# Performance work log

Measured on AMD Instinct MI355X. Metric: run time of the kernel, lower is better.

## Reference

```python
import jax, jax.numpy as jnp
import numpy as np

PH = PW = 5  # roi_size
EPS = 1e-5


def _conv1x1(x, w, b):
    # x: (B,Cin,H,W), w: (Cout,Cin)
    return jnp.einsum('bchw,oc->bohw', x, w) + b[None, :, None, None]


def _resize_ac(x, oh, ow):
    # F.interpolate bilinear, align_corners=True. x: (B,C,H,W)
    B, C, H, W = x.shape
    ys = jnp.linspace(0.0, H - 1.0, oh)
    xs = jnp.linspace(0.0, W - 1.0, ow)
    y0 = jnp.floor(ys).astype(jnp.int32); y1 = jnp.minimum(y0 + 1, H - 1)
    x0 = jnp.floor(xs).astype(jnp.int32); x1 = jnp.minimum(x0 + 1, W - 1)
    ly = (ys - y0)[:, None]; lx = (xs - x0)[None, :]
    v00 = x[:, :, y0[:, None], x0[None, :]]
    v01 = x[:, :, y0[:, None], x1[None, :]]
    v10 = x[:, :, y1[:, None], x0[None, :]]
    v11 = x[:, :, y1[:, None], x1[None, :]]
    return v00 * (1 - ly) * (1 - lx) + v01 * (1 - ly) * lx + v10 * ly * (1 - lx) + v11 * ly * lx


def _roi_align_one(feat, box):
    # torchvision RoIAlign, spatial_scale=1, sampling_ratio=1, aligned=False
    # feat: (C,H,W), box: (x1,y1,x2,y2)
    C, H, W = feat.shape
    bx1, by1, bx2, by2 = box[0], box[1], box[2], box[3]
    rw = jnp.maximum(bx2 - bx1, 1.0)
    rh = jnp.maximum(by2 - by1, 1.0)
    xs = bx1 + (jnp.arange(PW, dtype=feat.dtype) + 0.5) * (rw / PW)
    ys = by1 + (jnp.arange(PH, dtype=feat.dtype) + 0.5) * (rh / PH)
    yg = jnp.broadcast_to(ys[:, None], (PH, PW))
    xg = jnp.broadcast_to(xs[None, :], (PH, PW))
    valid = (yg >= -1.0) & (yg <= H) & (xg >= -1.0) & (xg <= W)
    y = jnp.clip(yg, 0.0, H - 1.0); x = jnp.clip(xg, 0.0, W - 1.0)
    y0 = jnp.floor(y).astype(jnp.int32); x0 = jnp.floor(x).astype(jnp.int32)
    y1i = jnp.minimum(y0 + 1, H - 1); x1i = jnp.minimum(x0 + 1, W - 1)
    ly = y - y0; lx = x - x0
    v = (feat[:, y0, x0] * (1 - ly) * (1 - lx) + feat[:, y0, x1i] * (1 - ly) * lx
         + feat[:, y1i, x0] * ly * (1 - lx) + feat[:, y1i, x1i] * ly * lx)
    return v * valid  # (C,PH,PW)


def _layernorm(x, w, b):
    mu = jnp.mean(x, -1, keepdims=True)
    var = jnp.var(x, -1, keepdims=True)
    return (x - mu) * jax.lax.rsqrt(var + EPS) * w + b


def setup_inputs() -> dict:
    key = jax.random.key(0)
    ks = jax.random.split(key, 16)
    B, G, NB, HF = 8, 8, 16, 28
    x4 = jax.random.normal(ks[0], (B, 1024, 14, 14), jnp.float32)
    x5 = jax.random.normal(ks[1], (B, 2048, 7, 7), jnp.float32)
    bx = jax.random.uniform(ks[2], (B, NB), minval=0.0, maxval=18.0)
    by = jax.random.uniform(ks[3], (B, NB), minval=0.0, maxval=18.0)
    bw = jax.random.uniform(ks[4], (B, NB), minval=3.0, maxval=10.0)
    bh = jax.random.uniform(ks[5], (B, NB), minval=3.0, maxval=10.0)
    boxes = jnp.stack([bx, by, jnp.minimum(bx + bw, 28.0), jnp.minimum(by + bh, 28.0)], -1)
    group = jax.random.randint(ks[6], (B, G, 2), 0, NB, jnp.int32)
    real_in_num = jnp.full((B,), G, jnp.int32)
    label_s = jax.random.randint(ks[7], (B, G), 0, 6, jnp.int64)
    label_s = jnp.where(jnp.arange(G)[None, :] % 3 == 0, -1, label_s)  # exercise both branches
    skeleton = jax.random.normal(ks[8], (B, G, HF, HF), jnp.float32)
    D = 1536 * PH * PW  # 38400
    return {
        'x4': x4, 'x5': x5, 'boxes': boxes, 'skeleton': skeleton,
        'group': group, 'real_in_num': real_in_num, 'label_s': label_s,
        'conv1_w': jax.random.normal(ks[9], (), jnp.float32) * 0.5,
        'conv1_b': jax.random.normal(ks[10], (), jnp.float32) * 0.1,
        'conv2_w': jax.random.normal(ks[11], (512, 1024), jnp.float32) * 0.03,
        'conv2_b': jnp.zeros((512,), jnp.float32),
        'conv3_w': jax.random.normal(ks[12], (1024, 2048), jnp.float32) * 0.02,
        'conv3_b': jnp.zeros((1024,), jnp.float32),
        'norm1_w': jnp.ones((D,), jnp.float32), 'norm1_b': jnp.zeros((D,), jnp.float32),
        'norm2_w': jnp.ones((512,), jnp.float32), 'norm2_b': jnp.zeros((512,), jnp.float32),
        'fc1_w': jax.random.normal(ks[13], (512, D), jnp.float32) * float(np.sqrt(2.0 / D)),
        'fc1_b': jnp.zeros((512,), jnp.float32),
        'fc2_w': jax.random.normal(ks[14], (6, 512), jnp.float32) * float(np.sqrt(2.0 / 512)),
        'fc2_b': jnp.zeros((6,), jnp.float32),
    }


def reference(x4, x5, boxes, skeleton, group, real_in_num, label_s,
              conv1_w, conv1_b, conv2_w, conv2_b, conv3_w, conv3_b,
              norm1_w, norm1_b, norm2_w, norm2_b, fc1_w, fc1_b, fc2_w, fc2_b):
    B, G = skeleton.shape[0], skeleton.shape[1]
    HF, WF = skeleton.shape[2], skeleton.shape[3]
    # backbone heads: 1x1 conv + bilinear upsample (align_corners=True), concat
    f4 = _resize_ac(_conv1x1(x4, conv2_w, conv2_b), HF, WF)   # (B,512,28,28)
    f5 = _resize_ac(_conv1x1(x5, conv3_w, conv3_b), HF, WF)   # (B,1024,28,28)
    app = jnp.concatenate([f4, f5], axis=1)                   # (B,1536,28,28)
    C = app.shape[1]
    # per-person pose gate: 1x1 conv (scalar on single channel) + sigmoid
    gate = jax.nn.sigmoid(skeleton * conv1_w + conv1_b)       # (B,G,28,28)
    gated = gate[:, :, None] * app[:, None]                   # (B,G,C,28,28)
    use_gate = (label_s != -1)[:, :, None, None, None]
    pose_feature = jnp.where(use_gate, gated, app[:, None])   # (B,G,C,28,28)
    # union box of the two interacting people (get_box_tensor)
    bidx = jnp.arange(B)[:, None]
    b1 = boxes[bidx, group[..., 0]]                           # (B,G,4)
    b2 = boxes[bidx, group[..., 1]]
    ub = jnp.stack([jnp.minimum(b1[..., 0], b2[..., 0]), jnp.minimum(b1[..., 1], b2[..., 1]),
                    jnp.maximum(b1[..., 2], b2[..., 2]), jnp.maximum(b1[..., 3], b2[..., 3])], -1)
    # batched RoIAlign over all N = B*G boxes
    feats = pose_feature.reshape(B * G, C, HF, WF)
    rois = jax.vmap(_roi_align_one)(feats, ub.reshape(B * G, 4))  # (N,C,5,5)
    sk = rois.reshape(B * G, -1)                              # (N,38400)
    sk = jax.nn.relu(_layernorm(sk, norm1_w, norm1_b))
    # dropout(p=0.9) is identity in eval mode
    sk = sk @ fc1_w.T + fc1_b
    sk = _layernorm(sk, norm2_w, norm2_b)
    score = sk @ fc2_w.T + fc2_b                              # (N,6)
    return score
```

## Files before the change

### kernel.cpp

```cpp
#include <hip/hip_runtime.h>
#include <math.h>

#define B8   8
#define HW4  196
#define HW5  49
#define HFW  28
#define NPIX 784
#define CAPP 1536
#define D1   38400
#define NR   64

typedef short short8 __attribute__((ext_vector_type(8)));
typedef short short4v __attribute__((ext_vector_type(4)));
typedef float floatx16 __attribute__((ext_vector_type(16)));

__device__ __forceinline__ unsigned short f2bf(float f) {
  unsigned u = __float_as_uint(f);
  u += 0x7FFF + ((u >> 16) & 1);
  return (unsigned short)(u >> 16);
}

struct Params {
  const float *x4, *x5, *boxes, *skel;
  const int *group, *label;
  const float *c1w, *c1b, *w2c, *b2c, *w3c, *b3c;
  const float *n1w, *n1b, *n2w, *n2b, *fw1, *fb1, *fw2, *fb2;
  float* out;
  unsigned short *x4T, *x5T, *sknT;
  float *f4T, *f5T, *tap4w, *tap5w, *descw, *roisP, *stats, *out1;
  int *tap4o, *tap5o, *desco;
};

struct Sh0 { float tile[6432]; };
struct GemmSh {
  unsigned short As[4096];
  unsigned short Bs[4096];
};
struct Sh2 {
  float cw4[16], cw5[16], wgs;
  int co4[16], co5[16];
  float red[8];
};
struct Sh3 { float tile[6424]; };
struct Sh5 { float red[8]; float red2[24]; };

__device__ __forceinline__ void gemm_unit(
    GemmSh& sh, const unsigned short* __restrict__ A, const float* __restrict__ Bw,
    float* __restrict__ C, int mt, int nt, int k0, int kchunk,
    int K, int N, int Mvalid, bool accum) {
  int t = threadIdx.x;
  int wave = t >> 6, lane = t & 63;
  int wm = wave & 1, wn = wave >> 1;
  const unsigned short* Aptr = A + (size_t)(mt * 64) * K + k0;
  const float* Bptr = Bw + (size_t)(nt * 64) * K + k0;

  int m0 = t >> 3, ka = (t & 7) * 8, koa = t & 7;
  int n0 = t >> 4, kbo = (t & 15) * 4, kob = (t & 15) >> 1, half = t & 1;

  short8 areg[2];
  float4 breg[4];
  floatx16 acc;
#pragma unroll
  for (int i = 0; i < 16; i++) acc[i] = 0.f;
  int nkb = kchunk >> 6;

  auto LOAD = [&](int j) {
    int kof = j * 64;
    areg[0] = *(const short8*)(Aptr + (size_t)m0 * K + kof + ka);
    areg[1] = *(const short8*)(Aptr + (size_t)(m0 + 32) * K + kof + ka);
#pragma unroll
    for (int i = 0; i < 4; i++)
      breg[i] = *(const float4*)(Bptr + (size_t)(n0 + 16 * i) * K + kof + kbo);
  };
  auto STORE = [&]() {
    *(short8*)&sh.As[koa * 512 + ((m0 ^ koa)) * 8] = areg[0];
    *(short8*)&sh.As[koa * 512 + (((m0 + 32) ^ koa)) * 8] = areg[1];
#pragma unroll
    for (int i = 0; i < 4; i++) {
      short4v v;
      v[0] = (short)f2bf(breg[i].x); v[1] = (short)f2bf(breg[i].y);
      v[2] = (short)f2bf(breg[i].z); v[3] = (short)f2bf(breg[i].w);
      int n = n0 + 16 * i;
      *(short4v*)&sh.Bs[kob * 512 + ((n ^ kob)) * 8 + half * 4] = v;
    }
  };

  LOAD(0);
  STORE();
  __syncthreads();

  for (int kb = 0; kb < nkb; kb++) {
    bool more = (kb + 1) < nkb;
    if (more) LOAD(kb + 1);
#pragma unroll
    for (int s = 0; s < 4; s++) {
      int ko = 2 * s + (lane >> 5);
      int am = wm * 32 + (lane & 31);
      int bn = wn * 32 + (lane & 31);
      short8 af = *(const short8*)&sh.As[ko * 512 + ((am ^ ko)) * 8];
      short8 bf = *(const short8*)&sh.Bs[ko * 512 + ((bn ^ ko)) * 8];
      acc = __builtin_amdgcn_mfma_f32_32x32x16_bf16(af, bf, acc, 0, 0, 0);
    }
    __syncthreads();
    if (more) {
      STORE();
      __syncthreads();
    }
  }

  int col = nt * 64 + wn * 32 + (lane & 31);
  int rbase = mt * 64 + wm * 32 + 4 * (lane >> 5);
  if (accum) {
#pragma unroll
    for (int reg = 0; reg < 16; reg++) {
      int row = rbase + (reg & 3) + 8 * (reg >> 2);
      if (row < Mvalid) atomicAdd(&C[(size_t)row * N + col], acc[reg]);
    }
  } else {
#pragma unroll
    for (int reg = 0; reg < 16; reg++) {
      int row = rbase + (reg & 3) + 8 * (reg >> 2);
      if (row < Mvalid) C[(size_t)row * N + col] = acc[reg];
    }
  }
}

__device__ __forceinline__ float gate_val(const float* sk, int yy, int xx,
                                          float c1w, float c1b, bool use) {
  if (!use) return 1.f;
  float z = sk[yy * HFW + xx] * c1w + c1b;
  return 1.f / (1.f + expf(-z));
}

__global__ __launch_bounds__(256, 4) void k_phase0(Params p) {
  __shared__ Sh0 sh;
  int bid = blockIdx.x, t = threadIdx.x, gb = gridDim.x;
  int gtid = bid * 256 + t;
  int nth = gb * 256;
  float4 z4 = make_float4(0.f, 0.f, 0.f, 0.f);
  for (int i = gtid; i < 319488; i += nth) ((float4*)p.f4T)[i] = z4;
  for (int i = gtid; i < 8192; i += nth) ((float4*)p.out1)[i] = z4;
  if (gtid < 128) p.stats[gtid] = 0.f;

  for (int u = bid; u < 836; u += gb) {
    __syncthreads();
    if (u < 256) {
      int b = u >> 5, cc = u & 31;
      for (int i = t; i < 32 * HW4; i += 256) {
        int c = i / HW4, hw = i - c * HW4;
        sh.tile[c * 201 + hw] = p.x4[((size_t)(b * 1024 + cc * 32 + c)) * HW4 + hw];
      }
      __syncthreads();
      for (int i = t; i < HW4 * 32; i += 256) {
        int hw = i >> 5, c = i & 31;
        p.x4T[((size_t)(b * HW4 + hw)) * 1024 + cc * 32 + c] = f2bf(sh.tile[c * 201 + hw]);
      }
    } else if (u < 768) {
      int u2 = u - 256;
      int b = u2 >> 6, cc = u2 & 63;
      for (int i = t; i < 32 * HW5; i += 256) {
        int c = i / HW5, hw = i - c * HW5;
        sh.tile[c * 51 + hw] = p.x5[((size_t)(b * 2048 + cc * 32 + c)) * HW5 + hw];
      }
      __syncthreads();
      for (int i = t; i < HW5 * 32; i += 256) {
        int hw = i >> 5, c = i & 31;
        p.x5T[((size_t)(b * HW5 + hw)) * 2048 + cc * 32 + c] = f2bf(sh.tile[c * 51 + hw]);
      }
    } else if (u < 832) {
      int bg = u - 768;
      if (t < 25) {
        int b = bg >> 3;
        int i1 = p.group[bg * 2 + 0], i2 = p.group[bg * 2 + 1];
        const float* bb1 = p.boxes + (size_t)(b * 16 + i1) * 4;
        const float* bb2 = p.boxes + (size_t)(b * 16 + i2) * 4;
        float ux1 = fminf(bb1[0], bb2[0]);
        float uy1 = fminf(bb1[1], bb2[1]);
        float ux2 = fmaxf(bb1[2], bb2[2]);
        float uy2 = fmaxf(bb1[3], bb2[3]);
        float rw = fmaxf(ux2 - ux1, 1.0f), rh = fmaxf(uy2 - uy1, 1.0f);
        int iy = t / 5, ix = t % 5;
        float sy = uy1 + (iy + 0.5f) * (rh * 0.2f);
        float sx = ux1 + (ix + 0.5f) * (rw * 0.2f);
        float valid = (sy >= -1.0f && sy <= 28.0f && sx >= -1.0f && sx <= 28.0f) ? 1.f : 0.f;
        float y = fminf(fmaxf(sy, 0.f), 27.f);
        float x = fminf(fmaxf(sx, 0.f), 27.f);
        int y0 = (int)floorf(y), x0 = (int)floorf(x);
        int y1 = min(y0 + 1, 27), x1 = min(x0 + 1, 27);
        float ly = y - (float)y0, lx = x - (float)x0;
        bool use = (p.label[bg] != -1);
        float c1w = p.c1w[0], c1b = p.c1b[0];
        const float* sk = p.skel + (size_t)bg * NPIX;
        int idx = (bg * 25 + t) * 4;
        p.descw[idx + 0] = (1.f - ly) * (1.f - lx) * valid * gate_val(sk, y0, x0, c1w, c1b, use);
        p.descw[idx + 1] = (1.f - ly) * lx * valid * gate_val(sk, y0, x1, c1w, c1b, use);
        p.descw[idx + 2] = ly * (1.f - lx) * valid * gate_val(sk, y1, x0, c1w, c1b, use);
        p.descw[idx + 3] = ly * lx * valid * gate_val(sk, y1, x1, c1w, c1b, use);
        p.desco[idx + 0] = y0 * HFW + x0;
        p.desco[idx + 1] = y0 * HFW + x1;
        p.desco[idx + 2] = y1 * HFW + x0;
        p.desco[idx + 3] = y1 * HFW + x1;
      }
    } else {
      int pix = (u - 832) * 196 + t;
      if (t < 196) {
        int y = pix / HFW, x = pix % HFW;
        {
          float sy = y * (13.0f / 27.0f), sx = x * (13.0f / 27.0f);
          int y0 = (int)sy, x0 = (int)sx;
          int y1 = min(y0 + 1, 13), x1 = min(x0 + 1, 13);
          float ly = sy - y0, lx = sx - x0;
          p.tap4o[pix * 4 + 0] = y0 * 14 + x0; p.tap4w[pix * 4 + 0] = (1.f - ly) * (1.f - lx);
          p.tap4o[pix * 4 + 1] = y0 * 14 + x1; p.tap4w[pix * 4 + 1] = (1.f - ly) * lx;
          p.tap4o[pix * 4 + 2] = y1 * 14 + x0; p.tap4w[pix * 4 + 2] = ly * (1.f - lx);
          p.tap4o[pix * 4 + 3] = y1 * 14 + x1; p.tap4w[pix * 4 + 3] = ly * lx;
        }
        {
          float sy = y * (6.0f / 27.0f), sx = x * (6.0f / 27.0f);
          int y0 = (int)sy, x0 = (int)sx;
          int y1 = min(y0 + 1, 6), x1 = min(x0 + 1, 6);
          float ly = sy - y0, lx = sx - x0;
          p.tap5o[pix * 4 + 0] = y0 * 7 + x0; p.tap5w[pix * 4 + 0] = (1.f - ly) * (1.f - lx);
          p.tap5o[pix * 4 + 1] = y0 * 7 + x1; p.tap5w[pix * 4 + 1] = (1.f - ly) * lx;
          p.tap5o[pix * 4 + 2] = y1 * 7 + x0; p.tap5w[pix * 4 + 2] = ly * (1.f - lx);
          p.tap5o[pix * 4 + 3] = y1 * 7 + x1; p.tap5w[pix * 4 + 3] = ly * lx;
        }
      }
    }
  }
}

__global__ __launch_bounds__(256, 4) void k_phase1(Params p) {
  __shared__ GemmSh sh;
  int bid = blockIdx.x, gb = gridDim.x;
  for (int u = bid; u < 1696; u += gb) {
    __syncthreads();
    if (u < 800) {
      int mt = u % 25, r = u / 25;
      int nt = r & 7, sp = r >> 3;
      gemm_unit(sh, p.x4T, p.w2c, p.f4T, mt, nt, sp * 256, 256, 1024, 512, 1568, true);
    } else {
      int u2 = u - 800;
      int mt = u2 % 7, r = u2 / 7;
      int nt = r & 15, sp = r >> 4;
      gemm_unit(sh, p.x5T, p.w3c, p.f5T, mt, nt, sp * 256, 256, 2048, 1024, 392, true);
    }
  }
}

__global__ __launch_bounds__(256, 4) void k_phase2(Params p) {
  __shared__ Sh2 sh;
  int bid = blockIdx.x, t = threadIdx.x, gb = gridDim.x;
  for (int u = bid; u < 1600; u += gb) {
    __syncthreads();
    int pp = u % 25, bg = u / 25, b = bg >> 3;
    int di = (bg * 25 + pp) * 4;
    if (t < 16) {
      int i = t >> 2, j = t & 3;
      float wg = p.descw[di + i];
      int pix = p.desco[di + i];
      sh.cw4[t] = wg * p.tap4w[pix * 4 + j];
      sh.co4[t] = (b * HW4 + p.tap4o[pix * 4 + j]) * 512;
      sh.cw5[t] = wg * p.tap5w[pix * 4 + j];
      sh.co5[t] = (b * HW5 + p.tap5o[pix * 4 + j]) * 1024;
    }
    if (t == 16) sh.wgs = p.descw[di] + p.descw[di + 1] + p.descw[di + 2] + p.descw[di + 3];
    __syncthreads();
    float w4r[16], w5r[16];
    int o4r[16], o5r[16];
    float wg = sh.wgs;
#pragma unroll
    for (int i = 0; i < 16; i++) {
      w4r[i] = sh.cw4[i]; o4r[i] = sh.co4[i];
      w5r[i] = sh.cw5[i]; o5r[i] = sh.co5[i];
    }
    float ls = 0.f, ls2 = 0.f;
    float* outp = p.roisP + (size_t)(bg * 25 + pp) * CAPP;
    for (int c = t; c < 512; c += 256) {
      float acc = wg * p.b2c[c];
#pragma unroll
      for (int i = 0; i < 16; i++) acc = fmaf(w4r[i], p.f4T[o4r[i] + c], acc);
      outp[c] = acc;
      ls += acc; ls2 = fmaf(acc, acc, ls2);
    }
    for (int c = t; c < 1024; c += 256) {
      float acc = wg * p.b3c[c];
#pragma unroll
      for (int i = 0; i < 16; i++) acc = fmaf(w5r[i], p.f5T[o5r[i] + c], acc);
      outp[512 + c] = acc;
      ls += acc; ls2 = fmaf(acc, acc, ls2);
    }
    for (int off = 32; off; off >>= 1) {
      ls += __shfl_down(ls, off);
      ls2 += __shfl_down(ls2, off);
    }
    int wv = t >> 6;
    if ((t & 63) == 0) { sh.red[wv] = ls; sh.red[4 + wv] = ls2; }
    __syncthreads();
    if (t == 0) {
      atomicAdd(&p.stats[bg * 2 + 0], sh.red[0] + sh.red[1] + sh.red[2] + sh.red[3]);
      atomicAdd(&p.stats[bg * 2 + 1], sh.red[4] + sh.red[5] + sh.red[6] + sh.red[7]);
    }
  }
}

__global__ __launch_bounds__(256, 4) void k_phase3(Params p) {
  __shared__ Sh3 sh;
  int bid = blockIdx.x, t = threadIdx.x, gb = gridDim.x;
  for (int u = bid; u < 384; u += gb) {
    __syncthreads();
    int r = u / 6, ch = u - r * 6;
    int c0 = ch * 256;
    float S = p.stats[r * 2], S2 = p.stats[r * 2 + 1];
    float mu = S * (1.f / D1);
    float var = S2 * (1.f / D1) - mu * mu;
    float rs = rsqrtf(var + 1e-5f);
    const float* rp = p.roisP + (size_t)r * 25 * CAPP + c0;
#pragma unroll
    for (int pp = 0; pp < 25; pp++)
      sh.tile[pp * 257 + t] = rp[(size_t)pp * CAPP + t];
    __syncthreads();
    unsigned short* op = p.sknT + (size_t)r * D1 + c0 * 25;
    const float* wv = p.n1w + c0 * 25;
    const float* bv = p.n1b + c0 * 25;
    for (int j = t; j < 6400; j += 256) {
      unsigned cc = (unsigned)j / 25u;
      unsigned pp = (unsigned)j - cc * 25u;
      float x = sh.tile[pp * 257 + cc];
      float v = fmaf((x - mu) * rs, wv[j], bv[j]);
      op[j] = f2bf(fmaxf(v, 0.f));
    }
  }
}

__global__ __launch_bounds__(256, 4) void k_phase4(Params p) {
  __shared__ GemmSh sh;
  int bid = blockIdx.x, gb = gridDim.x;
  for (int u = bid; u < 960; u += gb) {
    __syncthreads();
    int nt = u & 7, sp = u >> 3;
    gemm_unit(sh, p.sknT, p.fw1, p.out1, 0, nt, sp * 320, 320, 38400, 512, 64, true);
  }
}

__global__ __launch_bounds__(256, 4) void k_phase5(Params p) {
  __shared__ Sh5 sh;
  int bid = blockIdx.x, t = threadIdx.x, gb = gridDim.x;
  for (int r = bid; r < NR; r += gb) {
    __syncthreads();
    int j1 = t, j2 = t + 256;
    float v1 = p.out1[r * 512 + j1] + p.fb1[j1];
    float v2 = p.out1[r * 512 + j2] + p.fb1[j2];
    float s = v1 + v2, s2 = v1 * v1 + v2 * v2;
    for (int off = 32; off; off >>= 1) {
      s += __shfl_down(s, off);
      s2 += __shfl_down(s2, off);
    }
    int wv = t >> 6;
    if ((t & 63) == 0) { sh.red[wv] = s; sh.red[4 + wv] = s2; }
    __syncthreads();
    float S = sh.red[0] + sh.red[1] + sh.red[2] + sh.red[3];
    float S2 = sh.red[4] + sh.red[5] + sh.red[6] + sh.red[7];
    float mu = S / 512.f;
    float var = S2 / 512.f - mu * mu;
    float rs = rsqrtf(var + 1e-5f);
    float n1v = fmaf((v1 - mu) * rs, p.n2w[j1], p.n2b[j1]);
    float n2v = fmaf((v2 - mu) * rs, p.n2w[j2], p.n2b[j2]);
    float pm[6];
#pragma unroll
    for (int m = 0; m < 6; m++)
      pm[m] = n1v * p.fw2[m * 512 + j1] + n2v * p.fw2[m * 512 + j2];
#pragma unroll
    for (int m = 0; m < 6; m++)
      for (int off = 32; off; off >>= 1) pm[m] += __shfl_down(pm[m], off);
    if ((t & 63) == 0) {
#pragma unroll
      for (int m = 0; m < 6; m++) sh.red2[wv * 6 + m] = pm[m];
    }
    __syncthreads();
    if (t < 6)
      p.out[r * 6 + t] = sh.red2[t] + sh.red2[6 + t] + sh.red2[12 + t] +
                         sh.red2[18 + t] + p.fb2[t];
  }
}

extern "C" void kernel_launch(void* const* d_in, const int* in_sizes, int n_in,
                              void* d_out, int out_size, void* d_ws, size_t ws_size,
                              hipStream_t stream) {
  Params p;
  p.x4    = (const float*)d_in[0];
  p.x5    = (const float*)d_in[1];
  p.boxes = (const float*)d_in[2];
  p.skel  = (const float*)d_in[3];
  p.group = (const int*)d_in[4];
  p.label = (const int*)d_in[6];
  p.c1w   = (const float*)d_in[7];
  p.c1b   = (const float*)d_in[8];
  p.w2c   = (const float*)d_in[9];
  p.b2c   = (const float*)d_in[10];
  p.w3c   = (const float*)d_in[11];
  p.b3c   = (const float*)d_in[12];
  p.n1w   = (const float*)d_in[13];
  p.n1b   = (const float*)d_in[14];
  p.n2w   = (const float*)d_in[15];
  p.n2b   = (const float*)d_in[16];
  p.fw1   = (const float*)d_in[17];
  p.fb1   = (const float*)d_in[18];
  p.fw2   = (const float*)d_in[19];
  p.fb2   = (const float*)d_in[20];
  p.out   = (float*)d_out;

  float* ws = (float*)d_ws;
  p.x4T   = (unsigned short*)ws;
  p.x5T   = (unsigned short*)(ws + 819200);
  p.f4T   = ws + 1277952;
  p.f5T   = ws + 2097152;
  p.tap4w = ws + 2555904;
  p.tap4o = (int*)(ws + 2559040);
  p.tap5w = ws + 2562176;
  p.tap5o = (int*)(ws + 2565312);
  p.descw = ws + 2568448;
  p.desco = (int*)(ws + 2574848);
  p.roisP = ws + 2581248;
  p.stats = ws + 5038848;
  p.sknT  = (unsigned short*)(ws + 5038976);
  p.out1  = ws + 6267776;

  k_phase0<<<836,  256, 0, stream>>>(p);
  k_phase1<<<1696, 256, 0, stream>>>(p);
  k_phase2<<<1600, 256, 0, stream>>>(p);
  k_phase3<<<384,  256, 0, stream>>>(p);
  k_phase4<<<960,  256, 0, stream>>>(p);
  k_phase5<<<64,   256, 0, stream>>>(p);
}
```

Before: 242.0 us.

## Pre-convert conv weights to bf16 and remap block order for XCD locality

Converts the fp32 conv1x1 weights w2c and w3c to bf16 once, in phase 0, so the phase 1 GEMM loads bf16 B tiles directly instead of loading fp32 and converting in every tile. This halves B-operand global traffic and removes the repeated conversion work. It also permutes the work-unit index in phases 1, 2 and 4, (uu&7)*N + (uu>>3), so that neighbouring units land on the same XCD and share L2. The cost is an extra pass over about 12 MB of weights in phase 0 each call.

Measured after the change: 235.7 us (median of 3 runs). 1.03x faster.

```diff
diff --git a/kernel.cpp b/kernel.cpp
--- a/kernel.cpp
+++ b/kernel.cpp
@@ -26,7 +26,7 @@
   const float *c1w, *c1b, *w2c, *b2c, *w3c, *b3c;
   const float *n1w, *n1b, *n2w, *n2b, *fw1, *fb1, *fw2, *fb2;
   float* out;
-  unsigned short *x4T, *x5T, *sknT;
+  unsigned short *x4T, *x5T, *sknT, *w2cH, *w3cH;
   float *f4T, *f5T, *tap4w, *tap5w, *descw, *roisP, *stats, *out1;
   int *tap4o, *tap5o, *desco;
 };
@@ -44,20 +44,23 @@
 struct Sh3 { float tile[6424]; };
 struct Sh5 { float red[8]; float red2[24]; };
 
+template <bool BHALF>
 __device__ __forceinline__ void gemm_unit(
-    GemmSh& sh, const unsigned short* __restrict__ A, const float* __restrict__ Bw,
+    GemmSh& sh, const unsigned short* __restrict__ A, const void* __restrict__ Bw,
     float* __restrict__ C, int mt, int nt, int k0, int kchunk,
     int K, int N, int Mvalid, bool accum) {
   int t = threadIdx.x;
   int wave = t >> 6, lane = t & 63;
   int wm = wave & 1, wn = wave >> 1;
   const unsigned short* Aptr = A + (size_t)(mt * 64) * K + k0;
-  const float* Bptr = Bw + (size_t)(nt * 64) * K + k0;
+  const unsigned short* Bph = (const unsigned short*)Bw + (size_t)(nt * 64) * K + k0;
+  const float* Bpf = (const float*)Bw + (size_t)(nt * 64) * K + k0;
 
   int m0 = t >> 3, ka = (t & 7) * 8, koa = t & 7;
   int n0 = t >> 4, kbo = (t & 15) * 4, kob = (t & 15) >> 1, half = t & 1;
 
   short8 areg[2];
+  short8 bregh[2];
   float4 breg[4];
   floatx16 acc;
 #pragma unroll
@@ -68,20 +71,30 @@
     int kof = j * 64;
     areg[0] = *(const short8*)(Aptr + (size_t)m0 * K + kof + ka);
     areg[1] = *(const short8*)(Aptr + (size_t)(m0 + 32) * K + kof + ka);
-#pragma unroll
-    for (int i = 0; i < 4; i++)
-      breg[i] = *(const float4*)(Bptr + (size_t)(n0 + 16 * i) * K + kof + kbo);
+    if constexpr (BHALF) {
+      bregh[0] = *(const short8*)(Bph + (size_t)m0 * K + kof + ka);
+      bregh[1] = *(const short8*)(Bph + (size_t)(m0 + 32) * K + kof + ka);
+    } else {
+#pragma unroll
+      for (int i = 0; i < 4; i++)
+        breg[i] = *(const float4*)(Bpf + (size_t)(n0 + 16 * i) * K + kof + kbo);
+    }
   };
   auto STORE = [&]() {
     *(short8*)&sh.As[koa * 512 + ((m0 ^ koa)) * 8] = areg[0];
     *(short8*)&sh.As[koa * 512 + (((m0 + 32) ^ koa)) * 8] = areg[1];
-#pragma unroll
-    for (int i = 0; i < 4; i++) {
-      short4v v;
-      v[0] = (short)f2bf(breg[i].x); v[1] = (short)f2bf(breg[i].y);
-      v[2] = (short)f2bf(breg[i].z); v[3] = (short)f2bf(breg[i].w);
-      int n = n0 + 16 * i;
-      *(short4v*)&sh.Bs[kob * 512 + ((n ^ kob)) * 8 + half * 4] = v;
+    if constexpr (BHALF) {
+      *(short8*)&sh.Bs[koa * 512 + ((m0 ^ koa)) * 8] = bregh[0];
+      *(short8*)&sh.Bs[koa * 512 + (((m0 + 32) ^ koa)) * 8] = bregh[1];
+    } else {
+#pragma unroll
+      for (int i = 0; i < 4; i++) {
+        short4v v;
+        v[0] = (short)f2bf(breg[i].x); v[1] = (short)f2bf(breg[i].y);
+        v[2] = (short)f2bf(breg[i].z); v[3] = (short)f2bf(breg[i].w);
+        int n = n0 + 16 * i;
+        *(short4v*)&sh.Bs[kob * 512 + ((n ^ kob)) * 8 + half * 4] = v;
+      }
     }
   };
 
@@ -141,6 +154,20 @@
   for (int i = gtid; i < 319488; i += nth) ((float4*)p.f4T)[i] = z4;
   for (int i = gtid; i < 8192; i += nth) ((float4*)p.out1)[i] = z4;
   if (gtid < 128) p.stats[gtid] = 0.f;
+  for (int i = gtid; i < 131072; i += nth) {
+    float4 v = ((const float4*)p.w2c)[i];
+    short4v h;
+    h[0] = (short)f2bf(v.x); h[1] = (short)f2bf(v.y);
+    h[2] = (short)f2bf(v.z); h[3] = (short)f2bf(v.w);
+    *(short4v*)&p.w2cH[i * 4] = h;
+  }
+  for (int i = gtid; i < 524288; i += nth) {
+    float4 v = ((const float4*)p.w3c)[i];
+    short4v h;
+    h[0] = (short)f2bf(v.x); h[1] = (short)f2bf(v.y);
+    h[2] = (short)f2bf(v.z); h[3] = (short)f2bf(v.w);
+    *(short4v*)&p.w3cH[i * 4] = h;
+  }
 
   for (int u = bid; u < 836; u += gb) {
     __syncthreads();
@@ -233,17 +260,18 @@
 __global__ __launch_bounds__(256, 4) void k_phase1(Params p) {
   __shared__ GemmSh sh;
   int bid = blockIdx.x, gb = gridDim.x;
-  for (int u = bid; u < 1696; u += gb) {
+  for (int uu = bid; uu < 1696; uu += gb) {
+    int u = (uu & 7) * 212 + (uu >> 3);
     __syncthreads();
     if (u < 800) {
       int mt = u % 25, r = u / 25;
       int nt = r & 7, sp = r >> 3;
-      gemm_unit(sh, p.x4T, p.w2c, p.f4T, mt, nt, sp * 256, 256, 1024, 512, 1568, true);
+      gemm_unit<true>(sh, p.x4T, p.w2cH, p.f4T, mt, nt, sp * 256, 256, 1024, 512, 1568, true);
     } else {
       int u2 = u - 800;
       int mt = u2 % 7, r = u2 / 7;
       int nt = r & 15, sp = r >> 4;
-      gemm_unit(sh, p.x5T, p.w3c, p.f5T, mt, nt, sp * 256, 256, 2048, 1024, 392, true);
+      gemm_unit<true>(sh, p.x5T, p.w3cH, p.f5T, mt, nt, sp * 256, 256, 2048, 1024, 392, true);
     }
   }
 }
@@ -251,7 +279,8 @@
 __global__ __launch_bounds__(256, 4) void k_phase2(Params p) {
   __shared__ Sh2 sh;
   int bid = blockIdx.x, t = threadIdx.x, gb = gridDim.x;
-  for (int u = bid; u < 1600; u += gb) {
+  for (int uu = bid; uu < 1600; uu += gb) {
+    int u = (uu & 7) * 200 + (uu >> 3);
     __syncthreads();
     int pp = u % 25, bg = u / 25, b = bg >> 3;
     int di = (bg * 25 + pp) * 4;
@@ -336,10 +365,11 @@
 __global__ __launch_bounds__(256, 4) void k_phase4(Params p) {
   __shared__ GemmSh sh;
   int bid = blockIdx.x, gb = gridDim.x;
-  for (int u = bid; u < 960; u += gb) {
+  for (int uu = bid; uu < 960; uu += gb) {
+    int u = (uu & 7) * 120 + (uu >> 3);
     __syncthreads();
     int nt = u & 7, sp = u >> 3;
-    gemm_unit(sh, p.sknT, p.fw1, p.out1, 0, nt, sp * 320, 320, 38400, 512, 64, true);
+    gemm_unit<false>(sh, p.sknT, p.fw1, p.out1, 0, nt, sp * 320, 320, 38400, 512, 64, true);
   }
 }
 
@@ -425,6 +455,8 @@
   p.stats = ws + 5038848;
   p.sknT  = (unsigned short*)(ws + 5038976);
   p.out1  = ws + 6267776;
+  p.w2cH  = (unsigned short*)(ws + 6300544);
+  p.w3cH  = (unsigned short*)(ws + 6562688);
 
   k_phase0<<<836,  256, 0, stream>>>(p);
   k_phase1<<<1696, 256, 0, stream>>>(p);
```
